# Optimization experiments

Measured on AMD Instinct MI355X. Metric: run time of the kernel, lower is better.

Reference implementation:

```python
import jax, jax.numpy as jnp
import numpy as np

D_K = 16
TAU = 1.0


def gumbel_softmax_hard(logits, key, tau=TAU):
    # logits: [B, M]; straight-through hard gumbel-softmax along axis 1
    u = jax.random.uniform(key, logits.shape, minval=1e-10, maxval=1.0)
    g = -jnp.log(-jnp.log(u))
    y_soft = jax.nn.softmax((logits + g) / tau, axis=1)
    idx = jnp.argmax(y_soft, axis=1)
    y_hard = jax.nn.one_hot(idx, logits.shape[1], dtype=logits.dtype)
    return jax.lax.stop_gradient(y_hard - y_soft) + y_soft


def setup_inputs() -> dict:
    key = jax.random.key(0)
    k1, k2, k3, k4 = jax.random.split(key, 4)
    B, NR, NW, DR, DW = 32768, 5, 5, 512, 512
    q = jax.random.normal(k1, (B, NR, DR), dtype=jnp.float32)
    k = jax.random.normal(k2, (B, NW, DW), dtype=jnp.float32)
    # GroupLinearLayer weights: [num_blocks, d_in, d_k], init 0.01*randn (NPS convention)
    w_read = 0.01 * jax.random.normal(k3, (NR, DR, D_K), dtype=jnp.float32)
    w_write = 0.01 * jax.random.normal(k4, (NW, DW, D_K), dtype=jnp.float32)
    return {"q": q, "k": k, "w_read": w_read, "w_write": w_write}


def reference(q, k, w_read, w_write):
    temp = jnp.sqrt(jnp.asarray(D_K, dtype=q.dtype))
    # group-linear (block-diagonal) projections
    read = jnp.einsum('bnd,ndk->bnk', q, w_read)    # [B, NR, d_k]
    write = jnp.einsum('bmd,mdk->bmk', k, w_write)  # [B, NW, d_k]
    # scores for the first two read slots against all write slots
    scores_1 = jnp.einsum('bk,bmk->bm', read[:, 0], write) / temp  # [B, NW]
    scores_2 = jnp.einsum('bk,bmk->bm', read[:, 1], write) / temp  # [B, NW]
    g1 = gumbel_softmax_hard(scores_1, jax.random.key(42))
    g2 = gumbel_softmax_hard(scores_2, jax.random.key(43))
    return (g1, g2)
```

## Files before the change

kernel.cpp:

```cpp
#include <hip/hip_runtime.h>
#include <stdint.h>
#include <math.h>

#define NB    32768
#define NSLOT 5
#define DIM   512
#define DK    16

__device__ __forceinline__ uint32_t rotl32(uint32_t x, uint32_t r) {
  return (x << r) | (x >> (32u - r));
}

__device__ __forceinline__ void threefry2x32_20(uint32_t k0, uint32_t k1,
                                                uint32_t& x0, uint32_t& x1) {
  const uint32_t ks[3] = {k0, k1, k0 ^ k1 ^ 0x1BD11BDAu};
  const uint32_t rotA[4] = {13u, 15u, 26u, 6u};
  const uint32_t rotB[4] = {17u, 29u, 16u, 24u};
  x0 += ks[0];
  x1 += ks[1];
#pragma unroll
  for (int i = 0; i < 5; ++i) {
#pragma unroll
    for (int j = 0; j < 4; ++j) {
      uint32_t r = (i & 1) ? rotB[j] : rotA[j];
      x0 += x1;
      x1 = rotl32(x1, r);
      x1 ^= x0;
    }
    x0 += ks[(i + 1) % 3];
    x1 += ks[(i + 2) % 3] + (uint32_t)(i + 1);
  }
}

__device__ __forceinline__ uint32_t jax_random_bits_part(uint32_t key_lo, uint32_t i) {
  uint32_t x0 = 0u;
  uint32_t x1 = i;
  threefry2x32_20(0u, key_lo, x0, x1);
  return x0 ^ x1;
}

__global__ __launch_bounds__(256) void csa_kernel(
    const float* __restrict__ q,
    const float* __restrict__ kin,
    const float* __restrict__ wr,
    const float* __restrict__ ww,
    float* __restrict__ out)
{
  const int t  = threadIdx.x;
  const int kk = t & 15;
  const int bl = t >> 4;
  const int b  = blockIdx.x * 16 + bl;

  float acc[7];
#pragma unroll
  for (int s = 0; s < 7; ++s) acc[s] = 0.0f;

#pragma unroll
  for (int s = 0; s < 7; ++s) {
    const float* a;
    const float* w;
    if (s < 2) {
      a = q   + ((size_t)(b * NSLOT + s)) * DIM;
      w = wr  + (size_t)s * (DIM * DK) + kk;
    } else {
      a = kin + ((size_t)(b * NSLOT + (s - 2))) * DIM;
      w = ww  + (size_t)(s - 2) * (DIM * DK) + kk;
    }
    const float4* a4 = (const float4*)a;
    float sum = 0.0f;
#pragma unroll 4
    for (int d4 = 0; d4 < DIM / 4; ++d4) {
      float4 av = a4[d4];
      const float* wd = w + (size_t)d4 * 4 * DK;
      sum = fmaf(av.x, wd[0 * DK], sum);
      sum = fmaf(av.y, wd[1 * DK], sum);
      sum = fmaf(av.z, wd[2 * DK], sum);
      sum = fmaf(av.w, wd[3 * DK], sum);
    }
    acc[s] = sum;
  }

  float score[10];
#pragma unroll
  for (int n = 0; n < 2; ++n) {
#pragma unroll
    for (int m = 0; m < NSLOT; ++m) {
      float p = acc[n] * acc[2 + m];
      p += __shfl_xor(p, 1, 16);
      p += __shfl_xor(p, 2, 16);
      p += __shfl_xor(p, 4, 16);
      p += __shfl_xor(p, 8, 16);
      score[n * NSLOT + m] = p * 0.25f;
    }
  }

  if (kk < 2) {
    const int n = kk;
    const uint32_t key_lo = (n == 0) ? 42u : 43u;
    int best = 0;
    float bestv = -INFINITY;
#pragma unroll
    for (int m = 0; m < NSLOT; ++m) {
      uint32_t i = (uint32_t)(b * NSLOT + m);
      uint32_t bits = jax_random_bits_part(key_lo, i);
      float f = __uint_as_float((bits >> 9) | 0x3F800000u) - 1.0f;
      float u = fmaxf(1e-10f, f + 1e-10f);
      double tt = -log((double)u);
      float g = (float)(-log(tt));
      float z = score[n * NSLOT + m] + g;
      if (z > bestv) { bestv = z; best = m; }
    }
    float* o = out + (size_t)n * (NB * NSLOT) + (size_t)b * NSLOT;
#pragma unroll
    for (int m = 0; m < NSLOT; ++m) o[m] = (m == best) ? 1.0f : 0.0f;
  }
}

extern "C" void kernel_launch(void* const* d_in, const int* in_sizes, int n_in,
                              void* d_out, int out_size, void* d_ws, size_t ws_size,
                              hipStream_t stream) {
  const float* q  = (const float*)d_in[0];
  const float* k  = (const float*)d_in[1];
  const float* wr = (const float*)d_in[2];
  const float* ww = (const float*)d_in[3];
  float* out = (float*)d_out;

  dim3 grid(NB / 16);
  dim3 block(256);
  csa_kernel<<<grid, block, 0, stream>>>(q, k, wr, ww, out);
}
```

Measured before the change: 1.011 ms.

## Split projection work across d-quarters and k-quads with float4 weight loads

Each of the 16 threads per row now takes a quarter of the input dimension and computes four output columns, instead of one output column over the full dimension. Each thread reads only its own quarter of each activation row rather than the whole row, and weights are fetched as float4 vectors. Partial sums are combined with cross-lane shuffles before the score dot products. This cuts redundant activation reads and load instructions, at the cost of more shuffle reductions and more accumulator registers.

```diff
diff --git a/kernel.cpp b/kernel.cpp
--- a/kernel.cpp
+++ b/kernel.cpp
@@ -39,6 +39,12 @@
   return x0 ^ x1;
 }
 
+__device__ __forceinline__ float red_dq(float v) {
+  v += __shfl_xor(v, 4);
+  v += __shfl_xor(v, 8);
+  return v;
+}
+
 __global__ __launch_bounds__(256) void csa_kernel(
     const float* __restrict__ q,
     const float* __restrict__ kin,
@@ -46,71 +52,90 @@
     const float* __restrict__ ww,
     float* __restrict__ out)
 {
-  const int t  = threadIdx.x;
-  const int kk = t & 15;
-  const int bl = t >> 4;
-  const int b  = blockIdx.x * 16 + bl;
+  const int g   = blockIdx.x * 256 + threadIdx.x;
+  const int sub = g & 15;
+  const int row = g >> 4;
+  const int kkq = sub & 3;
+  const int dq  = sub >> 2;
+  const int dbase = dq * 128;
 
-  float acc[7];
+  float r[2][4];
 #pragma unroll
-  for (int s = 0; s < 7; ++s) acc[s] = 0.0f;
-
+  for (int n = 0; n < 2; ++n) {
+    const float4* a4 = (const float4*)(q + ((size_t)row * NSLOT + n) * DIM + dbase);
+    const float* wb = wr + (size_t)n * DIM * DK + (size_t)dbase * DK + kkq * 4;
+    float ax = 0.f, ay = 0.f, az = 0.f, aw = 0.f;
+#pragma unroll 4
+    for (int it = 0; it < 32; ++it) {
+      float4 av = a4[it];
+      float4 w0 = *(const float4*)(wb + (size_t)(it * 4 + 0) * DK);
+      float4 w1 = *(const float4*)(wb + (size_t)(it * 4 + 1) * DK);
+      float4 w2 = *(const float4*)(wb + (size_t)(it * 4 + 2) * DK);
+      float4 w3 = *(const float4*)(wb + (size_t)(it * 4 + 3) * DK);
+      ax = fmaf(av.x, w0.x, ax); ay = fmaf(av.x, w0.y, ay);
+      az = fmaf(av.x, w0.z, az); aw = fmaf(av.x, w0.w, aw);
+      ax = fmaf(av.y, w1.x, ax); ay = fmaf(av.y, w1.y, ay);
+      az = fmaf(av.y, w1.z, az); aw = fmaf(av.y, w1.w, aw);
+      ax = fmaf(av.z, w2.x, ax); ay = fmaf(av.z, w2.y, ay);
+      az = fmaf(av.z, w2.z, az); aw = fmaf(av.z, w2.w, aw);
+      ax = fmaf(av.w, w3.x, ax); ay = fmaf(av.w, w3.y, ay);
+      az = fmaf(av.w, w3.z, az); aw = fmaf(av.w, w3.w, aw);
+    }
+    r[n][0] = ax; r[n][1] = ay; r[n][2] = az; r[n][3] = aw;
+  }
 #pragma unroll
-  for (int s = 0; s < 7; ++s) {
-    const float* a;
-    const float* w;
-    if (s < 2) {
-      a = q   + ((size_t)(b * NSLOT + s)) * DIM;
-      w = wr  + (size_t)s * (DIM * DK) + kk;
-    } else {
-      a = kin + ((size_t)(b * NSLOT + (s - 2))) * DIM;
-      w = ww  + (size_t)(s - 2) * (DIM * DK) + kk;
-    }
-    const float4* a4 = (const float4*)a;
-    float sum = 0.0f;
-#pragma unroll 4
-    for (int d4 = 0; d4 < DIM / 4; ++d4) {
-      float4 av = a4[d4];
-      const float* wd = w + (size_t)d4 * 4 * DK;
-      sum = fmaf(av.x, wd[0 * DK], sum);
-      sum = fmaf(av.y, wd[1 * DK], sum);
-      sum = fmaf(av.z, wd[2 * DK], sum);
-      sum = fmaf(av.w, wd[3 * DK], sum);
-    }
-    acc[s] = sum;
-  }
+  for (int n = 0; n < 2; ++n)
+#pragma unroll
+    for (int j = 0; j < 4; ++j) r[n][j] = red_dq(r[n][j]);
 
   float score[10];
 #pragma unroll
-  for (int n = 0; n < 2; ++n) {
-#pragma unroll
-    for (int m = 0; m < NSLOT; ++m) {
-      float p = acc[n] * acc[2 + m];
-      p += __shfl_xor(p, 1, 16);
-      p += __shfl_xor(p, 2, 16);
-      p += __shfl_xor(p, 4, 16);
-      p += __shfl_xor(p, 8, 16);
-      score[n * NSLOT + m] = p * 0.25f;
+  for (int m = 0; m < NSLOT; ++m) {
+    const float4* a4 = (const float4*)(kin + ((size_t)row * NSLOT + m) * DIM + dbase);
+    const float* wb = ww + (size_t)m * DIM * DK + (size_t)dbase * DK + kkq * 4;
+    float ax = 0.f, ay = 0.f, az = 0.f, aw = 0.f;
+#pragma unroll 4
+    for (int it = 0; it < 32; ++it) {
+      float4 av = a4[it];
+      float4 w0 = *(const float4*)(wb + (size_t)(it * 4 + 0) * DK);
+      float4 w1 = *(const float4*)(wb + (size_t)(it * 4 + 1) * DK);
+      float4 w2 = *(const float4*)(wb + (size_t)(it * 4 + 2) * DK);
+      float4 w3 = *(const float4*)(wb + (size_t)(it * 4 + 3) * DK);
+      ax = fmaf(av.x, w0.x, ax); ay = fmaf(av.x, w0.y, ay);
+      az = fmaf(av.x, w0.z, az); aw = fmaf(av.x, w0.w, aw);
+      ax = fmaf(av.y, w1.x, ax); ay = fmaf(av.y, w1.y, ay);
+      az = fmaf(av.y, w1.z, az); aw = fmaf(av.y, w1.w, aw);
+      ax = fmaf(av.z, w2.x, ax); ay = fmaf(av.z, w2.y, ay);
+      az = fmaf(av.z, w2.z, az); aw = fmaf(av.z, w2.w, aw);
+      ax = fmaf(av.w, w3.x, ax); ay = fmaf(av.w, w3.y, ay);
+      az = fmaf(av.w, w3.z, az); aw = fmaf(av.w, w3.w, aw);
     }
+    float wc0 = red_dq(ax), wc1 = red_dq(ay), wc2 = red_dq(az), wc3 = red_dq(aw);
+    float p0 = r[0][0] * wc0 + r[0][1] * wc1 + r[0][2] * wc2 + r[0][3] * wc3;
+    float p1 = r[1][0] * wc0 + r[1][1] * wc1 + r[1][2] * wc2 + r[1][3] * wc3;
+    p0 += __shfl_xor(p0, 1); p0 += __shfl_xor(p0, 2);
+    p1 += __shfl_xor(p1, 1); p1 += __shfl_xor(p1, 2);
+    score[0 * NSLOT + m] = p0 * 0.25f;
+    score[1 * NSLOT + m] = p1 * 0.25f;
   }
 
-  if (kk < 2) {
-    const int n = kk;
+  if (sub < 2) {
+    const int n = sub;
     const uint32_t key_lo = (n == 0) ? 42u : 43u;
     int best = 0;
     float bestv = -INFINITY;
 #pragma unroll
     for (int m = 0; m < NSLOT; ++m) {
-      uint32_t i = (uint32_t)(b * NSLOT + m);
+      uint32_t i = (uint32_t)(row * NSLOT + m);
       uint32_t bits = jax_random_bits_part(key_lo, i);
       float f = __uint_as_float((bits >> 9) | 0x3F800000u) - 1.0f;
       float u = fmaxf(1e-10f, f + 1e-10f);
       double tt = -log((double)u);
-      float g = (float)(-log(tt));
-      float z = score[n * NSLOT + m] + g;
+      float gmb = (float)(-log(tt));
+      float z = score[n * NSLOT + m] + gmb;
       if (z > bestv) { bestv = z; best = m; }
     }
-    float* o = out + (size_t)n * (NB * NSLOT) + (size_t)b * NSLOT;
+    float* o = out + (size_t)n * (NB * NSLOT) + (size_t)row * NSLOT;
 #pragma unroll
     for (int m = 0; m < NSLOT; ++m) o[m] = (m == best) ? 1.0f : 0.0f;
   }
```

After: 838.6 us. -17.1%, faster.
